# Optimization experiments

Measured on AMD Instinct MI355X. Metric: run time of the kernel, lower is better.

## Reference

```python
import jax, jax.numpy as jnp
import numpy as np

NH = 12          # num_heads
EPS = 1e-6       # eps for LayerNorm and QK RMSNorm
THETA = 10000.0


def _layernorm(x):
    # WanLayerNorm: fp32 layer-norm, no affine
    x = x.astype(jnp.float32)
    m = x.mean(-1, keepdims=True)
    v = ((x - m) ** 2).mean(-1, keepdims=True)
    return (x - m) * jax.lax.rsqrt(v + EPS)


def _rmsnorm(x, g):
    # WanRMSNorm: fp32 rms-norm then scale by weight g
    x32 = x.astype(jnp.float32)
    return x32 * jax.lax.rsqrt((x32 * x32).mean(-1, keepdims=True) + EPS) * g


def _rope_cos_sin(T, H, W, head_dim):
    # Per-token 3D RoPE angle tables. head_dim=128 -> half=64 complex pairs,
    # split [22, 21, 21] across (T, H, W) axes, matching rope_params/_build_freqs.
    half = head_dim // 2
    p_t = half - 2 * (half // 3)
    p_h = half // 3
    p_w = half // 3

    def ang(L, h):
        inv = 1.0 / (THETA ** (np.arange(h, dtype=np.float64) / h))
        return np.outer(np.arange(L, dtype=np.float64), inv)  # [L, h]

    a_t = np.broadcast_to(ang(T, p_t)[:, None, None, :], (T, H, W, p_t))
    a_h = np.broadcast_to(ang(H, p_h)[None, :, None, :], (T, H, W, p_h))
    a_w = np.broadcast_to(ang(W, p_w)[None, None, :, :], (T, H, W, p_w))
    a = np.concatenate([a_t, a_h, a_w], axis=-1).reshape(T * H * W, half)
    return jnp.asarray(np.cos(a), jnp.float32), jnp.asarray(np.sin(a), jnp.float32)


def _rope_apply(x, cos, sin):
    # x: [B, S, n, d]; pairs are interleaved along last dim (view_as_complex of reshape(..., -1, 2))
    xr = x[..., 0::2]
    xi = x[..., 1::2]
    c = cos[None, :, None, :]
    s = sin[None, :, None, :]
    out_r = xr * c - xi * s
    out_i = xr * s + xi * c
    return jnp.stack([out_r, out_i], axis=-1).reshape(x.shape)


def setup_inputs() -> dict:
    key = jax.random.key(0)
    ks = jax.random.split(key, 8)
    B, C, T, H, W = 1, 1536, 8, 22, 22
    scale = 1.0 / np.sqrt(C)
    return {
        "x": jax.random.normal(ks[0], (B, C, T, H, W), jnp.float32),
        "Wq": jax.random.normal(ks[1], (C, C), jnp.float32) * scale,
        "bq": jnp.zeros((C,), jnp.float32),
        "Wk": jax.random.normal(ks[2], (C, C), jnp.float32) * scale,
        "bk": jnp.zeros((C,), jnp.float32),
        "Wv": jax.random.normal(ks[3], (C, C), jnp.float32) * scale,
        "bv": jnp.zeros((C,), jnp.float32),
        "Wo": jax.random.normal(ks[4], (C, C), jnp.float32) * scale,
        "bo": jnp.zeros((C,), jnp.float32),
        "gq": jnp.ones((C,), jnp.float32),
        "gk": jnp.ones((C,), jnp.float32),
    }


def reference(x, Wq, bq, Wk, bk, Wv, bv, Wo, bo, gq, gk):
    B, C, T, H, W = x.shape
    S = T * H * W
    n = NH
    d = C // n

    # [B, C, T, H, W] -> [B, S, C]
    x_in = jnp.transpose(x, (0, 2, 3, 4, 1)).reshape(B, S, C)
    xn = _layernorm(x_in)

    # QKV projections + QK RMSNorm
    q = _rmsnorm(xn @ Wq.T + bq, gq).reshape(B, S, n, d)
    k = _rmsnorm(xn @ Wk.T + bk, gk).reshape(B, S, n, d)
    v = (xn @ Wv.T + bv).reshape(B, S, n, d)

    # 3D RoPE on q, k
    cos, sin = _rope_cos_sin(T, H, W, d)
    q = _rope_apply(q, cos, sin)
    k = _rope_apply(k, cos, sin)

    # scaled dot-product attention (flash_attention with default 1/sqrt(d) scale)
    scale = 1.0 / jnp.sqrt(jnp.float32(d))
    logits = jnp.einsum("bqhd,bkhd->bhqk", q, k) * scale
    attn = jax.nn.softmax(logits, axis=-1)
    o = jnp.einsum("bhqk,bkhd->bqhd", attn, v).reshape(B, S, C)

    # output projection + residual
    y = x_in + (o @ Wo.T + bo)
    return jnp.transpose(y.reshape(B, T, H, W, C), (0, 4, 1, 2, 3))
```

## Files before the change

kernel.cpp:

```cpp
#include <hip/hip_runtime.h>

#define S_TOT 3872
#define C_DIM 1536
#define NHEAD 12
#define DHEAD 128
#define TT 8
#define HH 22
#define WW 22
#define NKT 61
#define NKT2 31

typedef __bf16 bf16x8 __attribute__((ext_vector_type(8)));
typedef float  f32x4  __attribute__((ext_vector_type(4)));
typedef unsigned short u16x8 __attribute__((ext_vector_type(8)));

__device__ __forceinline__ float bf2f(unsigned short u) {
    unsigned int v = ((unsigned int)u) << 16;
    float f; __builtin_memcpy(&f, &v, 4); return f;
}
__device__ __forceinline__ unsigned short f2bf(float f) {
    unsigned int u; __builtin_memcpy(&u, &f, 4);
    u += 0x7fffu + ((u >> 16) & 1u);
    return (unsigned short)(u >> 16);
}
__device__ __forceinline__ unsigned int pk2_trunc(float a, float b) {
    unsigned int ua, ub;
    __builtin_memcpy(&ua, &a, 4); __builtin_memcpy(&ub, &b, 4);
    return (ua >> 16) | (ub & 0xffff0000u);
}
__device__ __forceinline__ float ldin(const void* p, size_t i, int isf32) {
    if (isf32) return ((const float*)p)[i];
    return bf2f(((const unsigned short*)p)[i]);
}
__device__ __forceinline__ float fexp2(float x) {
#if __has_builtin(__builtin_amdgcn_exp2f)
    return __builtin_amdgcn_exp2f(x);
#else
    return exp2f(x);
#endif
}
__device__ __forceinline__ void async16(const void* g, void* l) {
    __builtin_amdgcn_global_load_lds(
        (const __attribute__((address_space(1))) unsigned int*)g,
        (__attribute__((address_space(3))) unsigned int*)l, 16, 0, 0);
}
__device__ __forceinline__ int xcd_swz(int bid, int nwg) {
    int q = nwg >> 3, r = nwg & 7;
    int xcd = bid & 7, i = bid >> 3;
    int base = (xcd < r) ? xcd * (q + 1) : r * (q + 1) + (xcd - r) * q;
    return base + i;
}

__global__ void detect_vecs(const unsigned short* __restrict__ x,
                            const void* p0, const void* p1, const void* p2,
                            const void* p3, const void* p4, const void* p5,
                            int* __restrict__ flag, unsigned short* __restrict__ vecs,
                            float* __restrict__ sumb, float* __restrict__ sumsqb) {
    __shared__ int cnt;
    if (threadIdx.x == 0) cnt = 0;
    __syncthreads();
    int c = 0;
    for (int i = 0; i < 8; ++i) {
        unsigned short u = x[threadIdx.x * 8 + i];
        int e = (u >> 7) & 0xFF;
        if (e >= 112 && e <= 143) c++;
    }
    atomicAdd(&cnt, c);
    for (int j = threadIdx.x; j < S_TOT; j += 256) {
        sumb[j] = 0.f; sumsqb[j] = 0.f;
    }
    __syncthreads();
    int isf32 = (cnt >= 1900) ? 0 : 1;
    if (threadIdx.x == 0) *flag = isf32;
    const void* ps[6] = {p0, p1, p2, p3, p4, p5};
    for (int v = 0; v < 6; ++v)
        for (int j = threadIdx.x; j < C_DIM; j += 256)
            vecs[v * C_DIM + j] = f2bf(ldin(ps[v], j, isf32));
}

__global__ __launch_bounds__(256) void wconv4(const void* __restrict__ s0,
                                              const void* __restrict__ s1,
                                              const void* __restrict__ s2,
                                              const void* __restrict__ s3,
                                              const int* __restrict__ flag,
                                              unsigned short* __restrict__ d0,
                                              unsigned short* __restrict__ d1,
                                              unsigned short* __restrict__ d2,
                                              unsigned short* __restrict__ d3) {
    const void* srcs[4] = {s0, s1, s2, s3};
    unsigned short* dsts[4] = {d0, d1, d2, d3};
    const void* src = srcs[blockIdx.y];
    unsigned short* dst = dsts[blockIdx.y];
    size_t i = ((size_t)blockIdx.x * 256 + threadIdx.x) * 8;
    if (*flag) {
        const float* s = (const float*)src + i;
        float4 a = *(const float4*)s, b = *(const float4*)(s + 4);
        u16x8 o;
        o[0]=f2bf(a.x); o[1]=f2bf(a.y); o[2]=f2bf(a.z); o[3]=f2bf(a.w);
        o[4]=f2bf(b.x); o[5]=f2bf(b.y); o[6]=f2bf(b.z); o[7]=f2bf(b.w);
        *(u16x8*)(dst + i) = o;
    } else {
        *(u16x8*)(dst + i) = *(const u16x8*)((const unsigned short*)src + i);
    }
}

__global__ __launch_bounds__(256) void ln_stats(const void* __restrict__ x,
                                                const int* __restrict__ flag,
                                                float* __restrict__ sumb,
                                                float* __restrict__ sumsqb) {
    int isf32 = *flag;
    int sl = threadIdx.x & 63, cg = threadIdx.x >> 6;
    int s = blockIdx.x * 64 + sl;
    int cbase = blockIdx.y * 384;
    float sum = 0.f, sumsq = 0.f;
    if (s < S_TOT) {
        for (int c = cbase + cg; c < cbase + 384; c += 4) {
            float v = ldin(x, (size_t)c * S_TOT + s, isf32);
            sum += v; sumsq += v * v;
        }
    }
    __shared__ float r0[4][64], r1[4][64];
    r0[cg][sl] = sum; r1[cg][sl] = sumsq;
    __syncthreads();
    if (cg == 0 && s < S_TOT) {
        float st = r0[0][sl] + r0[1][sl] + r0[2][sl] + r0[3][sl];
        float sq = r1[0][sl] + r1[1][sl] + r1[2][sl] + r1[3][sl];
        atomicAdd(&sumb[s], st);
        atomicAdd(&sumsqb[s], sq);
    }
}

__global__ __launch_bounds__(256) void ln_norm_t(const void* __restrict__ x,
                                                 const int* __restrict__ flag,
                                                 const float* __restrict__ sumb,
                                                 const float* __restrict__ sumsqb,
                                                 unsigned short* __restrict__ xn) {
    int isf32 = *flag;
    __shared__ float tile[32][33];
    int s0 = blockIdx.x * 32, c0 = blockIdx.y * 32;
    int tx = threadIdx.x, ty = threadIdx.y;
    for (int r = 0; r < 4; ++r) {
        int cl = ty + 8 * r;
        tile[cl][tx] = ldin(x, (size_t)(c0 + cl) * S_TOT + (s0 + tx), isf32);
    }
    __syncthreads();
    for (int r = 0; r < 4; ++r) {
        int sl = ty + 8 * r;
        int s = s0 + sl, c = c0 + tx;
        float m = sumb[s] * (1.0f / C_DIM);
        float var = sumsqb[s] * (1.0f / C_DIM) - m * m;
        float rstd = rsqrtf(var + 1e-6f);
        xn[(size_t)s * C_DIM + c] = f2bf((tile[tx][sl] - m) * rstd);
    }
}

template<int BN>
__global__ __launch_bounds__(256, 3) void gemm2p(const unsigned short* __restrict__ A,
                                                 const unsigned short* __restrict__ W,
                                                 const unsigned short* __restrict__ bias,
                                                 unsigned short* __restrict__ D0,
                                                 unsigned short* __restrict__ D1,
                                                 unsigned short* __restrict__ DT,
                                                 int nsplit, int ntrans) {
    constexpr int NGRP = 8 + BN / 16;
    constexpr int GPW  = NGRP / 4;
    __shared__ __align__(16) unsigned short As[2][128 * 32];
    __shared__ __align__(16) unsigned short Bs[2][BN * 32];
    int nwg = gridDim.x * gridDim.y;
    int wg  = xcd_swz(blockIdx.y * gridDim.x + blockIdx.x, nwg);
    int m0 = (wg % gridDim.x) * 128, n0 = (wg / gridDim.x) * BN;
    int tid = threadIdx.x;
    int wave = tid >> 6, lane = tid & 63;
    int lm = lane & 15, lq = lane >> 4;
    int wr = wave >> 1, wc = wave & 1;
    int srow = lane >> 2, scol = (lane & 3) * 8;

    f32x4 acc[4][BN / 32];
    #pragma unroll
    for (int a = 0; a < 4; ++a)
        #pragma unroll
        for (int b = 0; b < BN / 32; ++b) acc[a][b] = (f32x4){0.f, 0.f, 0.f, 0.f};

    #pragma unroll
    for (int t = 0; t < GPW; ++t) {
        int g = wave * GPW + t;
        if (g < 8) {
            int am = m0 + g * 16 + srow; if (am > S_TOT - 1) am = S_TOT - 1;
            async16(A + (size_t)am * C_DIM + scol, (char*)As[0] + g * 1024);
        } else {
            int bn = n0 + (g - 8) * 16 + srow;
            async16(W + (size_t)bn * C_DIM + scol, (char*)Bs[0] + (g - 8) * 1024);
        }
    }
    int cur = 0;
    for (int k0 = 0; k0 < C_DIM; k0 += 32) {
        int kn = k0 + 32;
        if (kn < C_DIM) {
            #pragma unroll
            for (int t = 0; t < GPW; ++t) {
                int g = wave * GPW + t;
                if (g < 8) {
                    int am = m0 + g * 16 + srow; if (am > S_TOT - 1) am = S_TOT - 1;
                    async16(A + (size_t)am * C_DIM + kn + scol, (char*)As[cur ^ 1] + g * 1024);
                } else {
                    int bn = n0 + (g - 8) * 16 + srow;
                    async16(W + (size_t)bn * C_DIM + kn + scol, (char*)Bs[cur ^ 1] + (g - 8) * 1024);
                }
            }
            asm volatile("s_waitcnt vmcnt(%0)" :: "i"(GPW) : "memory");
        } else {
            asm volatile("s_waitcnt vmcnt(0)" ::: "memory");
        }
        __builtin_amdgcn_sched_barrier(0);
        __builtin_amdgcn_s_barrier();
        __builtin_amdgcn_sched_barrier(0);

        bf16x8 af[4], bf[BN / 32];
        #pragma unroll
        for (int mb = 0; mb < 4; ++mb)
            af[mb] = *(const bf16x8*)((const char*)As[cur] + (wr * 64 + mb * 16 + lm) * 64 + lq * 16);
        #pragma unroll
        for (int nb = 0; nb < BN / 32; ++nb)
            bf[nb] = *(const bf16x8*)((const char*)Bs[cur] + (wc * (BN / 2) + nb * 16 + lm) * 64 + lq * 16);
        #pragma unroll
        for (int mb = 0; mb < 4; ++mb)
            #pragma unroll
            for (int nb = 0; nb < BN / 32; ++nb)
                acc[mb][nb] = __builtin_amdgcn_mfma_f32_16x16x32_bf16(af[mb], bf[nb], acc[mb][nb], 0, 0, 0);

        __builtin_amdgcn_sched_barrier(0);
        __builtin_amdgcn_s_barrier();
        __builtin_amdgcn_sched_barrier(0);
        cur ^= 1;
    }

    #pragma unroll
    for (int mb = 0; mb < 4; ++mb) {
        #pragma unroll
        for (int nb = 0; nb < BN / 32; ++nb) {
            int gn = n0 + wc * (BN / 2) + nb * 16 + lm;
            float bv = bf2f(bias[gn]);
            if (gn >= ntrans) {
                int gm0 = m0 + wr * 64 + mb * 16 + lq * 4;
                if (gm0 < S_TOT) {
                    ushort4 pk;
                    pk.x = f2bf(acc[mb][nb][0] + bv);
                    pk.y = f2bf(acc[mb][nb][1] + bv);
                    pk.z = f2bf(acc[mb][nb][2] + bv);
                    pk.w = f2bf(acc[mb][nb][3] + bv);
                    *(ushort4*)(DT + (size_t)(gn - ntrans) * S_TOT + gm0) = pk;
                }
            } else {
                unsigned short* dst = (gn < nsplit) ? D0 : D1;
                int cn = (gn < nsplit) ? gn : gn - nsplit;
                #pragma unroll
                for (int r = 0; r < 4; ++r) {
                    int gm = m0 + wr * 64 + mb * 16 + lq * 4 + r;
                    if (gm < S_TOT) dst[(size_t)gm * C_DIM + cn] = f2bf(acc[mb][nb][r] + bv);
                }
            }
        }
    }
}

__global__ __launch_bounds__(256) void rope2(unsigned short* __restrict__ qbuf,
                                             unsigned short* __restrict__ kbuf,
                                             const unsigned short* __restrict__ gq,
                                             const unsigned short* __restrict__ gk,
                                             float qsc) {
    int s = blockIdx.x;
    unsigned short* row = (blockIdx.y ? kbuf : qbuf) + (size_t)s * C_DIM;
    const unsigned short* g = blockIdx.y ? gk : gq;
    float premul = blockIdx.y ? 1.0f : qsc;
    int tid = threadIdx.x;
    float ss = 0.f;
    for (int i = 0; i < 6; ++i) {
        float v = bf2f(row[tid + 256 * i]);
        ss += v * v;
    }
    for (int off = 32; off; off >>= 1) ss += __shfl_down(ss, off, 64);
    __shared__ float wsum[4];
    __shared__ float scale_sh;
    if ((tid & 63) == 0) wsum[tid >> 6] = ss;
    __syncthreads();
    if (tid == 0) {
        float tot = wsum[0] + wsum[1] + wsum[2] + wsum[3];
        scale_sh = rsqrtf(tot * (1.0f / C_DIM) + 1e-6f) * premul;
    }
    __syncthreads();
    float scale = scale_sh;

    int t  = s / (HH * WW);
    int rm = s % (HH * WW);
    int hh = rm / WW, ww = rm % WW;

    float e[3][2];
    int cols[3];
    for (int i = 0; i < 3; ++i) {
        int p = tid + 256 * i;
        int j = p & 63;
        int col0 = (p >> 6) * DHEAD + 2 * j;
        cols[i] = col0;
        float e0 = bf2f(row[col0])     * scale * bf2f(g[col0]);
        float e1 = bf2f(row[col0 + 1]) * scale * bf2f(g[col0 + 1]);
        float pos, fr;
        if (j < 22)       { pos = (float)t;  fr = (float)j        * (1.0f / 22.0f); }
        else if (j < 43)  { pos = (float)hh; fr = (float)(j - 22) * (1.0f / 21.0f); }
        else              { pos = (float)ww; fr = (float)(j - 43) * (1.0f / 21.0f); }
        float ang = pos * expf(fr * -9.210340371976184f);
        float c = cosf(ang), sn = sinf(ang);
        e[i][0] = e0 * c - e1 * sn;
        e[i][1] = e0 * sn + e1 * c;
    }
    for (int i = 0; i < 3; ++i) {
        row[cols[i]]     = f2bf(e[i][0]);
        row[cols[i] + 1] = f2bf(e[i][1]);
    }
}

__global__ __launch_bounds__(256, 2) void attn_mfma(const unsigned short* __restrict__ q,
                                                    const unsigned short* __restrict__ kp,
                                                    const unsigned short* __restrict__ vt,
                                                    unsigned short* __restrict__ o) {
    __shared__ __align__(16) unsigned char Ks[32768];
    __shared__ __align__(16) unsigned char Vs[32768];
    __shared__ __align__(16) unsigned char Ps[16384];

    int bid = xcd_swz(blockIdx.x, NHEAD * NKT);
    int h  = bid / NKT;
    int qt = bid % NKT;
    int q0 = qt * 64;
    int tid = threadIdx.x;
    int wave = tid >> 6, lane = tid & 63;
    int lm = lane & 15, lq = lane >> 4;

    bf16x8 qf[4];
    {
        int qr = q0 + wave * 16 + lm; if (qr >= S_TOT) qr = S_TOT - 1;
        const unsigned short* qptr = q + (size_t)qr * C_DIM + h * DHEAD + lq * 8;
        #pragma unroll
        for (int kc = 0; kc < 4; ++kc) qf[kc] = *(const bf16x8*)(qptr + kc * 32);
    }

    int krow = lane >> 4;
    int kcolA = ((lane & 15) ^ krow) * 8;
    int kcolB = ((lane & 15) ^ (4 + krow)) * 8;
    int vdr = lane >> 4;

    int sxor  = (lm & 7) << 4;
    int psxor = lm << 4;
    int ksoff[8], kqoff[4];
    #pragma unroll
    for (int nt = 0; nt < 8; ++nt) ksoff[nt] = (nt * 4 + (lm >> 2)) * 1024 + (lm & 3) * 256;
    #pragma unroll
    for (int kc = 0; kc < 4; ++kc) kqoff[kc] = (kc * 4 + lq) * 16;

    f32x4 oacc[8];
    #pragma unroll
    for (int i = 0; i < 8; ++i) oacc[i] = (f32x4){0.f, 0.f, 0.f, 0.f};
    float m_run = -__builtin_inff();
    float l_run = 0.f;

    for (int kt = 0; kt < NKT2; ++kt) {
        int k0 = kt * 128;
        #pragma unroll
        for (int t = 0; t < 8; ++t) {
            int g = wave * 8 + t;
            int grow = k0 + g * 4 + krow; if (grow > S_TOT - 1) grow = S_TOT - 1;
            async16(kp + (size_t)grow * C_DIM + h * DHEAD + ((t & 1) ? kcolB : kcolA),
                    Ks + g * 1024);
        }
        #pragma unroll
        for (int t = 0; t < 8; ++t) {
            int g = wave * 8 + t;
            int vslot = (lane & 15) ^ ((g & 3) * 4 + vdr);
            int vcol = k0 + vslot * 8; if (vcol > S_TOT - 8) vcol = S_TOT - 8;
            async16(vt + (size_t)(h * DHEAD + g * 4 + vdr) * S_TOT + vcol,
                    Vs + g * 1024);
        }
        __syncthreads();

        f32x4 sacc[8];
        #pragma unroll
        for (int nt = 0; nt < 8; ++nt) sacc[nt] = (f32x4){0.f, 0.f, 0.f, 0.f};
        #pragma unroll
        for (int kc = 0; kc < 4; ++kc)
            #pragma unroll
            for (int nt = 0; nt < 8; ++nt) {
                bf16x8 kf = *(const bf16x8*)(Ks + ((ksoff[nt] + kqoff[kc]) ^ sxor));
                sacc[nt] = __builtin_amdgcn_mfma_f32_16x16x32_bf16(kf, qf[kc], sacc[nt], 0, 0, 0);
            }
        if (kt == NKT2 - 1) {
            #pragma unroll
            for (int nt = 0; nt < 8; ++nt)
                #pragma unroll
                for (int r = 0; r < 4; ++r)
                    if (k0 + nt * 16 + lq * 4 + r >= S_TOT) sacc[nt][r] = -__builtin_inff();
        }
        float mtr[8];
        #pragma unroll
        for (int nt = 0; nt < 8; ++nt)
            mtr[nt] = fmaxf(fmaxf(sacc[nt][0], sacc[nt][1]),
                            fmaxf(sacc[nt][2], sacc[nt][3]));
        float pmax = fmaxf(fmaxf(fmaxf(mtr[0], mtr[1]), fmaxf(mtr[2], mtr[3])),
                           fmaxf(fmaxf(mtr[4], mtr[5]), fmaxf(mtr[6], mtr[7])));
        int defer = __all(pmax - m_run <= 8.0f);
        if (!defer) {
            float rmax = fmaxf(pmax, __shfl_xor(pmax, 16, 64));
            rmax = fmaxf(rmax, __shfl_xor(rmax, 32, 64));
            float mn = fmaxf(m_run, rmax);
            float alpha = fexp2(m_run - mn);
            l_run *= alpha;
            #pragma unroll
            for (int i = 0; i < 8; ++i)
                #pragma unroll
                for (int r = 0; r < 4; ++r) oacc[i][r] *= alpha;
            m_run = mn;
        }
        float rtot = 0.f;
        #pragma unroll
        for (int nt = 0; nt < 8; ++nt) {
            float p0 = fexp2(sacc[nt][0] - m_run);
            float p1 = fexp2(sacc[nt][1] - m_run);
            float p2 = fexp2(sacc[nt][2] - m_run);
            float p3 = fexp2(sacc[nt][3] - m_run);
            sacc[nt][0] = p0; sacc[nt][1] = p1;
            sacc[nt][2] = p2; sacc[nt][3] = p3;
            rtot += (p0 + p1) + (p2 + p3);
        }
        l_run += rtot;
        #pragma unroll
        for (int nt = 0; nt < 8; ++nt) {
            uint2 pk;
            pk.x = pk2_trunc(sacc[nt][0], sacc[nt][1]);
            pk.y = pk2_trunc(sacc[nt][2], sacc[nt][3]);
            *(uint2*)(Ps + (wave * 4096 + lm * 256 + ((nt * 32 + lq * 8) ^ psxor))) = pk;
        }
        #pragma unroll
        for (int kc = 0; kc < 4; ++kc) {
            bf16x8 pf = *(const bf16x8*)(Ps + (wave * 4096 + lm * 256 + ((kc * 64 + lq * 16) ^ psxor)));
            #pragma unroll
            for (int mt = 0; mt < 8; ++mt) {
                bf16x8 vf = *(const bf16x8*)(Vs + ((mt * 16 + lm) * 256 + ((kc * 64 + lq * 16) ^ psxor)));
                oacc[mt] = __builtin_amdgcn_mfma_f32_16x16x32_bf16(vf, pf, oacc[mt], 0, 0, 0);
            }
        }
        __syncthreads();
    }
    l_run += __shfl_xor(l_run, 16, 64);
    l_run += __shfl_xor(l_run, 32, 64);
    int qrow = q0 + wave * 16 + lm;
    if (qrow < S_TOT) {
        float inv = 1.0f / l_run;
        #pragma unroll
        for (int mt = 0; mt < 8; ++mt) {
            ushort4 pk;
            pk.x = f2bf(oacc[mt][0] * inv);
            pk.y = f2bf(oacc[mt][1] * inv);
            pk.z = f2bf(oacc[mt][2] * inv);
            pk.w = f2bf(oacc[mt][3] * inv);
            *(ushort4*)(o + (size_t)qrow * C_DIM + h * DHEAD + mt * 16 + lq * 4) = pk;
        }
    }
}

__global__ __launch_bounds__(256) void resid_t(const unsigned short* __restrict__ proj,
                                               const void* __restrict__ x,
                                               const int* __restrict__ flag,
                                               void* __restrict__ out) {
    int isf32 = *flag;
    __shared__ float tile[32][33];
    int s0 = blockIdx.x * 32, c0 = blockIdx.y * 32;
    int tx = threadIdx.x, ty = threadIdx.y;
    for (int r = 0; r < 4; ++r) {
        int sl = ty + 8 * r;
        tile[sl][tx] = bf2f(proj[(size_t)(s0 + sl) * C_DIM + (c0 + tx)]);
    }
    __syncthreads();
    for (int r = 0; r < 4; ++r) {
        int cl = ty + 8 * r;
        size_t idx = (size_t)(c0 + cl) * S_TOT + (s0 + tx);
        float val = ldin(x, idx, isf32) + tile[tx][cl];
        if (isf32) ((float*)out)[idx] = val;
        else       ((unsigned short*)out)[idx] = f2bf(val);
    }
}

extern "C" void kernel_launch(void* const* d_in, const int* in_sizes, int n_in,
                              void* d_out, int out_size, void* d_ws, size_t ws_size,
                              hipStream_t stream) {
    const void* x  = d_in[0];
    const void* Wq = d_in[1];
    const void* bq = d_in[2];
    const void* Wk = d_in[3];
    const void* bk = d_in[4];
    const void* Wv = d_in[5];
    const void* bv = d_in[6];
    const void* Wo = d_in[7];
    const void* bo = d_in[8];
    const void* gq = d_in[9];
    const void* gk = d_in[10];

    char* ws = (char*)d_ws;
    size_t off = 0;
    auto alloc = [&](size_t bytes) -> char* {
        char* p = ws + off;
        off += (bytes + 255) & ~(size_t)255;
        return p;
    };
    const size_t SC = (size_t)S_TOT * C_DIM;
    const size_t WSZ = (size_t)C_DIM * C_DIM * 2;
    unsigned short* xn   = (unsigned short*)alloc(SC * 2);
    unsigned short* qb   = (unsigned short*)alloc(SC * 2);
    unsigned short* kb   = (unsigned short*)alloc(SC * 2);
    unsigned short* Ws0  = (unsigned short*)alloc(WSZ);
    unsigned short* Ws1  = (unsigned short*)alloc(WSZ);
    unsigned short* Ws2  = (unsigned short*)alloc(WSZ);
    unsigned short* Ws3  = (unsigned short*)alloc(WSZ);
    unsigned short* vecs = (unsigned short*)alloc((size_t)6 * C_DIM * 2);
    float* sumb          = (float*)alloc((size_t)S_TOT * 4);
    float* sumsqb        = (float*)alloc((size_t)S_TOT * 4);
    int*   flag          = (int*)alloc(256);
    unsigned short* Vt   = (unsigned short*)d_out;
    unsigned short* ob   = xn;
    unsigned short* proj = qb;

    (void)Ws1; (void)Ws2;

    unsigned short* bo_b = vecs + 3 * C_DIM;
    unsigned short* gq_b = vecs + 4 * C_DIM;
    unsigned short* gk_b = vecs + 5 * C_DIM;

    const float QSC = 0.12751745f;

    dim3 t328(32, 8);
    dim3 tgrid(S_TOT / 32, C_DIM / 32);
    dim3 qkvgrid(31, 36);
    dim3 ogrid(31, 24);
    dim3 wgrid((C_DIM * C_DIM) / 2048, 4);
    dim3 sgrid(NKT, 4);
    dim3 rgrid(S_TOT, 2);

    detect_vecs<<<1, 256, 0, stream>>>((const unsigned short*)x, bq, bk, bv, bo, gq, gk,
                                       flag, vecs, sumb, sumsqb);
    wconv4<<<wgrid, 256, 0, stream>>>(Wq, Wk, Wv, Wo, flag, Ws0, Ws1, Ws2, Ws3);
    ln_stats<<<sgrid, 256, 0, stream>>>(x, flag, sumb, sumsqb);
    ln_norm_t<<<tgrid, t328, 0, stream>>>(x, flag, sumb, sumsqb, xn);

    gemm2p<128><<<qkvgrid, 256, 0, stream>>>(xn, Ws0, vecs, qb, kb, Vt, C_DIM, 2 * C_DIM);
    rope2<<<rgrid, 256, 0, stream>>>(qb, kb, gq_b, gk_b, QSC);

    attn_mfma<<<NHEAD * NKT, 256, 0, stream>>>(qb, kb, Vt, ob);

    gemm2p<64><<<ogrid, 256, 0, stream>>>(ob, Ws3, bo_b, proj, proj, proj, 1 << 30, 1 << 30);
    resid_t<<<tgrid, t328, 0, stream>>>(proj, x, flag, d_out);
}
```

Baseline: 500.0 us.

## Software-pipeline K/V async loads in attention and widen QKV GEMM tile

The attention loop now prefetches the next K tile right after the QK^T MFMAs and the next V tile right after the PV MFMAs. Explicit vmcnt waits and raw barriers replace the full __syncthreads, so global loads overlap compute instead of stalling at the top of each iteration. Separately, the QKV GEMM switches from a 128-wide to a 192-wide column tile, with a correspondingly smaller grid. The load pipelining relies on a hand-counted vmcnt(8), which risks races if the outstanding-load count does not match what the compiler emits, and the wider tile may reduce occupancy.

```diff
diff --git a/kernel.cpp b/kernel.cpp
--- a/kernel.cpp
+++ b/kernel.cpp
@@ -361,24 +361,40 @@
     float m_run = -__builtin_inff();
     float l_run = 0.f;
 
+#define STAGE_K(KT) do {                                                    \
+        int k0s = (KT) * 128;                                               \
+        _Pragma("unroll")                                                   \
+        for (int t = 0; t < 8; ++t) {                                       \
+            int g = wave * 8 + t;                                           \
+            int grow = k0s + g * 4 + krow; if (grow > S_TOT - 1) grow = S_TOT - 1; \
+            async16(kp + (size_t)grow * C_DIM + h * DHEAD + ((t & 1) ? kcolB : kcolA), \
+                    Ks + g * 1024);                                         \
+        } } while (0)
+#define STAGE_V(KT) do {                                                    \
+        int k0s = (KT) * 128;                                               \
+        _Pragma("unroll")                                                   \
+        for (int t = 0; t < 8; ++t) {                                       \
+            int g = wave * 8 + t;                                           \
+            int vslot = (lane & 15) ^ ((g & 3) * 4 + vdr);                  \
+            int vcol = k0s + vslot * 8; if (vcol > S_TOT - 8) vcol = S_TOT - 8; \
+            async16(vt + (size_t)(h * DHEAD + g * 4 + vdr) * S_TOT + vcol,  \
+                    Vs + g * 1024);                                         \
+        } } while (0)
+#define RAW_BARRIER() do {                                                  \
+        __builtin_amdgcn_sched_barrier(0);                                  \
+        __builtin_amdgcn_s_barrier();                                       \
+        __builtin_amdgcn_sched_barrier(0);                                  \
+    } while (0)
+
+    STAGE_K(0);
+    STAGE_V(0);
+
     for (int kt = 0; kt < NKT2; ++kt) {
         int k0 = kt * 128;
-        #pragma unroll
-        for (int t = 0; t < 8; ++t) {
-            int g = wave * 8 + t;
-            int grow = k0 + g * 4 + krow; if (grow > S_TOT - 1) grow = S_TOT - 1;
-            async16(kp + (size_t)grow * C_DIM + h * DHEAD + ((t & 1) ? kcolB : kcolA),
-                    Ks + g * 1024);
-        }
-        #pragma unroll
-        for (int t = 0; t < 8; ++t) {
-            int g = wave * 8 + t;
-            int vslot = (lane & 15) ^ ((g & 3) * 4 + vdr);
-            int vcol = k0 + vslot * 8; if (vcol > S_TOT - 8) vcol = S_TOT - 8;
-            async16(vt + (size_t)(h * DHEAD + g * 4 + vdr) * S_TOT + vcol,
-                    Vs + g * 1024);
-        }
-        __syncthreads();
+        int ktn = (kt + 1 < NKT2) ? kt + 1 : NKT2 - 1;
+
+        asm volatile("s_waitcnt vmcnt(8)" ::: "memory");
+        RAW_BARRIER();
 
         f32x4 sacc[8];
         #pragma unroll
@@ -390,6 +406,10 @@
                 bf16x8 kf = *(const bf16x8*)(Ks + ((ksoff[nt] + kqoff[kc]) ^ sxor));
                 sacc[nt] = __builtin_amdgcn_mfma_f32_16x16x32_bf16(kf, qf[kc], sacc[nt], 0, 0, 0);
             }
+
+        RAW_BARRIER();
+        STAGE_K(ktn);
+
         if (kt == NKT2 - 1) {
             #pragma unroll
             for (int nt = 0; nt < 8; ++nt)
@@ -436,6 +456,10 @@
             pk.y = pk2_trunc(sacc[nt][2], sacc[nt][3]);
             *(uint2*)(Ps + (wave * 4096 + lm * 256 + ((nt * 32 + lq * 8) ^ psxor))) = pk;
         }
+
+        asm volatile("s_waitcnt vmcnt(8)" ::: "memory");
+        RAW_BARRIER();
+
         #pragma unroll
         for (int kc = 0; kc < 4; ++kc) {
             bf16x8 pf = *(const bf16x8*)(Ps + (wave * 4096 + lm * 256 + ((kc * 64 + lq * 16) ^ psxor)));
@@ -445,8 +469,13 @@
                 oacc[mt] = __builtin_amdgcn_mfma_f32_16x16x32_bf16(vf, pf, oacc[mt], 0, 0, 0);
             }
         }
-        __syncthreads();
-    }
+
+        RAW_BARRIER();
+        STAGE_V(ktn);
+    }
+#undef STAGE_K
+#undef STAGE_V
+#undef RAW_BARRIER
     l_run += __shfl_xor(l_run, 16, 64);
     l_run += __shfl_xor(l_run, 32, 64);
     int qrow = q0 + wave * 16 + lm;
@@ -535,7 +564,7 @@
 
     dim3 t328(32, 8);
     dim3 tgrid(S_TOT / 32, C_DIM / 32);
-    dim3 qkvgrid(31, 36);
+    dim3 qkvgrid(31, 24);
     dim3 ogrid(31, 24);
     dim3 wgrid((C_DIM * C_DIM) / 2048, 4);
     dim3 sgrid(NKT, 4);
@@ -547,7 +576,7 @@
     ln_stats<<<sgrid, 256, 0, stream>>>(x, flag, sumb, sumsqb);
     ln_norm_t<<<tgrid, t328, 0, stream>>>(x, flag, sumb, sumsqb, xn);
 
-    gemm2p<128><<<qkvgrid, 256, 0, stream>>>(xn, Ws0, vecs, qb, kb, Vt, C_DIM, 2 * C_DIM);
+    gemm2p<192><<<qkvgrid, 256, 0, stream>>>(xn, Ws0, vecs, qb, kb, Vt, C_DIM, 2 * C_DIM);
     rope2<<<rgrid, 256, 0, stream>>>(qb, kb, gq_b, gk_b, QSC);
 
     attn_mfma<<<NHEAD * NKT, 256, 0, stream>>>(qb, kb, Vt, ob);
```

New measurement: 484.8 us. 1.03x faster.

## Restructure attention to 2 waves with 32 query rows each, 64-key tiles

Applied to the files above, without the earlier changes.

The attention kernel now runs 128 threads per block, and each wave handles two 16-row query groups. Each K/V fragment read from shared memory feeds two MFMAs, which raises reuse per LDS read. The key tile shrinks from 128 to 64, so LDS use drops and more blocks may fit per CU, at the cost of more loop iterations and barriers and higher register pressure. Separately, the QKV GEMM tile width changes from 128 to 192, with the grid adjusted to match.

```diff
diff --git a/kernel.cpp b/kernel.cpp
--- a/kernel.cpp
+++ b/kernel.cpp
@@ -8,7 +8,6 @@
 #define HH 22
 #define WW 22
 #define NKT 61
-#define NKT2 31
 
 typedef __bf16 bf16x8 __attribute__((ext_vector_type(8)));
 typedef float  f32x4  __attribute__((ext_vector_type(4)));
@@ -318,13 +317,13 @@
     }
 }
 
-__global__ __launch_bounds__(256, 2) void attn_mfma(const unsigned short* __restrict__ q,
+__global__ __launch_bounds__(128, 2) void attn_mfma(const unsigned short* __restrict__ q,
                                                     const unsigned short* __restrict__ kp,
                                                     const unsigned short* __restrict__ vt,
                                                     unsigned short* __restrict__ o) {
-    __shared__ __align__(16) unsigned char Ks[32768];
-    __shared__ __align__(16) unsigned char Vs[32768];
-    __shared__ __align__(16) unsigned char Ps[16384];
+    __shared__ __align__(16) unsigned char Ks[16384];
+    __shared__ __align__(16) unsigned char Vs[16384];
+    __shared__ __align__(16) unsigned char Ps[8192];
 
     int bid = xcd_swz(blockIdx.x, NHEAD * NKT);
     int h  = bid / NKT;
@@ -334,132 +333,149 @@
     int wave = tid >> 6, lane = tid & 63;
     int lm = lane & 15, lq = lane >> 4;
 
-    bf16x8 qf[4];
-    {
-        int qr = q0 + wave * 16 + lm; if (qr >= S_TOT) qr = S_TOT - 1;
+    bf16x8 qf[2][4];
+    #pragma unroll
+    for (int g = 0; g < 2; ++g) {
+        int qr = q0 + wave * 32 + g * 16 + lm; if (qr >= S_TOT) qr = S_TOT - 1;
         const unsigned short* qptr = q + (size_t)qr * C_DIM + h * DHEAD + lq * 8;
         #pragma unroll
-        for (int kc = 0; kc < 4; ++kc) qf[kc] = *(const bf16x8*)(qptr + kc * 32);
+        for (int kc = 0; kc < 4; ++kc) qf[g][kc] = *(const bf16x8*)(qptr + kc * 32);
     }
 
     int krow = lane >> 4;
     int kcolA = ((lane & 15) ^ krow) * 8;
     int kcolB = ((lane & 15) ^ (4 + krow)) * 8;
-    int vdr = lane >> 4;
-
-    int sxor  = (lm & 7) << 4;
-    int psxor = lm << 4;
-    int ksoff[8], kqoff[4];
-    #pragma unroll
-    for (int nt = 0; nt < 8; ++nt) ksoff[nt] = (nt * 4 + (lm >> 2)) * 1024 + (lm & 3) * 256;
+    int vr8 = lane >> 3;
+    int vslot = (lane & 7) ^ vr8;
+
+    int sxor = (lm & 7) << 4;
+    int ksoff[4], kqoff[4];
+    #pragma unroll
+    for (int nt = 0; nt < 4; ++nt) ksoff[nt] = (nt * 4 + (lm >> 2)) * 1024 + (lm & 3) * 256;
     #pragma unroll
     for (int kc = 0; kc < 4; ++kc) kqoff[kc] = (kc * 4 + lq) * 16;
 
-    f32x4 oacc[8];
-    #pragma unroll
-    for (int i = 0; i < 8; ++i) oacc[i] = (f32x4){0.f, 0.f, 0.f, 0.f};
-    float m_run = -__builtin_inff();
-    float l_run = 0.f;
-
-    for (int kt = 0; kt < NKT2; ++kt) {
-        int k0 = kt * 128;
+    f32x4 oacc[2][8];
+    #pragma unroll
+    for (int g = 0; g < 2; ++g)
+        #pragma unroll
+        for (int i = 0; i < 8; ++i) oacc[g][i] = (f32x4){0.f, 0.f, 0.f, 0.f};
+    float m_run[2] = {-__builtin_inff(), -__builtin_inff()};
+    float l_run[2] = {0.f, 0.f};
+
+    for (int kt = 0; kt < NKT; ++kt) {
+        int k0 = kt * 64;
         #pragma unroll
         for (int t = 0; t < 8; ++t) {
             int g = wave * 8 + t;
             int grow = k0 + g * 4 + krow; if (grow > S_TOT - 1) grow = S_TOT - 1;
-            async16(kp + (size_t)grow * C_DIM + h * DHEAD + ((t & 1) ? kcolB : kcolA),
+            async16(kp + (size_t)grow * C_DIM + h * DHEAD + ((g & 1) ? kcolB : kcolA),
                     Ks + g * 1024);
         }
-        #pragma unroll
-        for (int t = 0; t < 8; ++t) {
-            int g = wave * 8 + t;
-            int vslot = (lane & 15) ^ ((g & 3) * 4 + vdr);
+        {
             int vcol = k0 + vslot * 8; if (vcol > S_TOT - 8) vcol = S_TOT - 8;
-            async16(vt + (size_t)(h * DHEAD + g * 4 + vdr) * S_TOT + vcol,
-                    Vs + g * 1024);
+            #pragma unroll
+            for (int t = 0; t < 8; ++t) {
+                int g = wave * 8 + t;
+                async16(vt + (size_t)(h * DHEAD + g * 8 + vr8) * S_TOT + vcol,
+                        Vs + g * 1024);
+            }
         }
         __syncthreads();
 
-        f32x4 sacc[8];
-        #pragma unroll
-        for (int nt = 0; nt < 8; ++nt) sacc[nt] = (f32x4){0.f, 0.f, 0.f, 0.f};
+        f32x4 sacc[2][4];
+        #pragma unroll
+        for (int g = 0; g < 2; ++g)
+            #pragma unroll
+            for (int nt = 0; nt < 4; ++nt) sacc[g][nt] = (f32x4){0.f, 0.f, 0.f, 0.f};
         #pragma unroll
         for (int kc = 0; kc < 4; ++kc)
             #pragma unroll
-            for (int nt = 0; nt < 8; ++nt) {
+            for (int nt = 0; nt < 4; ++nt) {
                 bf16x8 kf = *(const bf16x8*)(Ks + ((ksoff[nt] + kqoff[kc]) ^ sxor));
-                sacc[nt] = __builtin_amdgcn_mfma_f32_16x16x32_bf16(kf, qf[kc], sacc[nt], 0, 0, 0);
-            }
-        if (kt == NKT2 - 1) {
-            #pragma unroll
-            for (int nt = 0; nt < 8; ++nt)
+                sacc[0][nt] = __builtin_amdgcn_mfma_f32_16x16x32_bf16(kf, qf[0][kc], sacc[0][nt], 0, 0, 0);
+                sacc[1][nt] = __builtin_amdgcn_mfma_f32_16x16x32_bf16(kf, qf[1][kc], sacc[1][nt], 0, 0, 0);
+            }
+        if (kt == NKT - 1) {
+            #pragma unroll
+            for (int g = 0; g < 2; ++g)
                 #pragma unroll
-                for (int r = 0; r < 4; ++r)
-                    if (k0 + nt * 16 + lq * 4 + r >= S_TOT) sacc[nt][r] = -__builtin_inff();
-        }
-        float mtr[8];
-        #pragma unroll
-        for (int nt = 0; nt < 8; ++nt)
-            mtr[nt] = fmaxf(fmaxf(sacc[nt][0], sacc[nt][1]),
-                            fmaxf(sacc[nt][2], sacc[nt][3]));
-        float pmax = fmaxf(fmaxf(fmaxf(mtr[0], mtr[1]), fmaxf(mtr[2], mtr[3])),
-                           fmaxf(fmaxf(mtr[4], mtr[5]), fmaxf(mtr[6], mtr[7])));
-        int defer = __all(pmax - m_run <= 8.0f);
-        if (!defer) {
-            float rmax = fmaxf(pmax, __shfl_xor(pmax, 16, 64));
-            rmax = fmaxf(rmax, __shfl_xor(rmax, 32, 64));
-            float mn = fmaxf(m_run, rmax);
-            float alpha = fexp2(m_run - mn);
-            l_run *= alpha;
-            #pragma unroll
-            for (int i = 0; i < 8; ++i)
+                for (int nt = 0; nt < 4; ++nt)
+                    #pragma unroll
+                    for (int r = 0; r < 4; ++r)
+                        if (k0 + nt * 16 + lq * 4 + r >= S_TOT) sacc[g][nt][r] = -__builtin_inff();
+        }
+        #pragma unroll
+        for (int g = 0; g < 2; ++g) {
+            float mtr[4];
+            #pragma unroll
+            for (int nt = 0; nt < 4; ++nt)
+                mtr[nt] = fmaxf(fmaxf(sacc[g][nt][0], sacc[g][nt][1]),
+                                fmaxf(sacc[g][nt][2], sacc[g][nt][3]));
+            float pmax = fmaxf(fmaxf(mtr[0], mtr[1]), fmaxf(mtr[2], mtr[3]));
+            int defer = __all(pmax - m_run[g] <= 8.0f);
+            if (!defer) {
+                float rmax = fmaxf(pmax, __shfl_xor(pmax, 16, 64));
+                rmax = fmaxf(rmax, __shfl_xor(rmax, 32, 64));
+                float mn = fmaxf(m_run[g], rmax);
+                float alpha = fexp2(m_run[g] - mn);
+                l_run[g] *= alpha;
                 #pragma unroll
-                for (int r = 0; r < 4; ++r) oacc[i][r] *= alpha;
-            m_run = mn;
-        }
-        float rtot = 0.f;
-        #pragma unroll
-        for (int nt = 0; nt < 8; ++nt) {
-            float p0 = fexp2(sacc[nt][0] - m_run);
-            float p1 = fexp2(sacc[nt][1] - m_run);
-            float p2 = fexp2(sacc[nt][2] - m_run);
-            float p3 = fexp2(sacc[nt][3] - m_run);
-            sacc[nt][0] = p0; sacc[nt][1] = p1;
-            sacc[nt][2] = p2; sacc[nt][3] = p3;
-            rtot += (p0 + p1) + (p2 + p3);
-        }
-        l_run += rtot;
-        #pragma unroll
-        for (int nt = 0; nt < 8; ++nt) {
-            uint2 pk;
-            pk.x = pk2_trunc(sacc[nt][0], sacc[nt][1]);
-            pk.y = pk2_trunc(sacc[nt][2], sacc[nt][3]);
-            *(uint2*)(Ps + (wave * 4096 + lm * 256 + ((nt * 32 + lq * 8) ^ psxor))) = pk;
-        }
-        #pragma unroll
-        for (int kc = 0; kc < 4; ++kc) {
-            bf16x8 pf = *(const bf16x8*)(Ps + (wave * 4096 + lm * 256 + ((kc * 64 + lq * 16) ^ psxor)));
+                for (int i = 0; i < 8; ++i)
+                    #pragma unroll
+                    for (int r = 0; r < 4; ++r) oacc[g][i][r] *= alpha;
+                m_run[g] = mn;
+            }
+            float rsn[4];
+            #pragma unroll
+            for (int nt = 0; nt < 4; ++nt) {
+                float p0 = fexp2(sacc[g][nt][0] - m_run[g]);
+                float p1 = fexp2(sacc[g][nt][1] - m_run[g]);
+                float p2 = fexp2(sacc[g][nt][2] - m_run[g]);
+                float p3 = fexp2(sacc[g][nt][3] - m_run[g]);
+                sacc[g][nt][0] = p0; sacc[g][nt][1] = p1;
+                sacc[g][nt][2] = p2; sacc[g][nt][3] = p3;
+                rsn[nt] = (p0 + p1) + (p2 + p3);
+            }
+            l_run[g] += (rsn[0] + rsn[1]) + (rsn[2] + rsn[3]);
+            #pragma unroll
+            for (int nt = 0; nt < 4; ++nt) {
+                uint2 pk;
+                pk.x = pk2_trunc(sacc[g][nt][0], sacc[g][nt][1]);
+                pk.y = pk2_trunc(sacc[g][nt][2], sacc[g][nt][3]);
+                *(uint2*)(Ps + (wave * 4096 + g * 2048 + lm * 128 + ((nt * 32 + lq * 8) ^ sxor))) = pk;
+            }
+        }
+        #pragma unroll
+        for (int kc = 0; kc < 2; ++kc) {
+            bf16x8 pf0 = *(const bf16x8*)(Ps + (wave * 4096 + lm * 128 + ((kc * 64 + lq * 16) ^ sxor)));
+            bf16x8 pf1 = *(const bf16x8*)(Ps + (wave * 4096 + 2048 + lm * 128 + ((kc * 64 + lq * 16) ^ sxor)));
             #pragma unroll
             for (int mt = 0; mt < 8; ++mt) {
-                bf16x8 vf = *(const bf16x8*)(Vs + ((mt * 16 + lm) * 256 + ((kc * 64 + lq * 16) ^ psxor)));
-                oacc[mt] = __builtin_amdgcn_mfma_f32_16x16x32_bf16(vf, pf, oacc[mt], 0, 0, 0);
+                bf16x8 vf = *(const bf16x8*)(Vs + ((mt * 16 + lm) * 128 + ((kc * 64 + lq * 16) ^ sxor)));
+                oacc[0][mt] = __builtin_amdgcn_mfma_f32_16x16x32_bf16(vf, pf0, oacc[0][mt], 0, 0, 0);
+                oacc[1][mt] = __builtin_amdgcn_mfma_f32_16x16x32_bf16(vf, pf1, oacc[1][mt], 0, 0, 0);
             }
         }
         __syncthreads();
     }
-    l_run += __shfl_xor(l_run, 16, 64);
-    l_run += __shfl_xor(l_run, 32, 64);
-    int qrow = q0 + wave * 16 + lm;
-    if (qrow < S_TOT) {
-        float inv = 1.0f / l_run;
-        #pragma unroll
-        for (int mt = 0; mt < 8; ++mt) {
-            ushort4 pk;
-            pk.x = f2bf(oacc[mt][0] * inv);
-            pk.y = f2bf(oacc[mt][1] * inv);
-            pk.z = f2bf(oacc[mt][2] * inv);
-            pk.w = f2bf(oacc[mt][3] * inv);
-            *(ushort4*)(o + (size_t)qrow * C_DIM + h * DHEAD + mt * 16 + lq * 4) = pk;
+    #pragma unroll
+    for (int g = 0; g < 2; ++g) {
+        float lt = l_run[g];
+        lt += __shfl_xor(lt, 16, 64);
+        lt += __shfl_xor(lt, 32, 64);
+        int qrow = q0 + wave * 32 + g * 16 + lm;
+        if (qrow < S_TOT) {
+            float inv = 1.0f / lt;
+            #pragma unroll
+            for (int mt = 0; mt < 8; ++mt) {
+                ushort4 pk;
+                pk.x = f2bf(oacc[g][mt][0] * inv);
+                pk.y = f2bf(oacc[g][mt][1] * inv);
+                pk.z = f2bf(oacc[g][mt][2] * inv);
+                pk.w = f2bf(oacc[g][mt][3] * inv);
+                *(ushort4*)(o + (size_t)qrow * C_DIM + h * DHEAD + mt * 16 + lq * 4) = pk;
+            }
         }
     }
 }
@@ -535,7 +551,7 @@
 
     dim3 t328(32, 8);
     dim3 tgrid(S_TOT / 32, C_DIM / 32);
-    dim3 qkvgrid(31, 36);
+    dim3 qkvgrid(31, 24);
     dim3 ogrid(31, 24);
     dim3 wgrid((C_DIM * C_DIM) / 2048, 4);
     dim3 sgrid(NKT, 4);
@@ -547,10 +563,10 @@
     ln_stats<<<sgrid, 256, 0, stream>>>(x, flag, sumb, sumsqb);
     ln_norm_t<<<tgrid, t328, 0, stream>>>(x, flag, sumb, sumsqb, xn);
 
-    gemm2p<128><<<qkvgrid, 256, 0, stream>>>(xn, Ws0, vecs, qb, kb, Vt, C_DIM, 2 * C_DIM);
+    gemm2p<192><<<qkvgrid, 256, 0, stream>>>(xn, Ws0, vecs, qb, kb, Vt, C_DIM, 2 * C_DIM);
     rope2<<<rgrid, 256, 0, stream>>>(qb, kb, gq_b, gk_b, QSC);
 
-    attn_mfma<<<NHEAD * NKT, 256, 0, stream>>>(qb, kb, Vt, ob);
+    attn_mfma<<<NHEAD * NKT, 128, 0, stream>>>(qb, kb, Vt, ob);
 
     gemm2p<64><<<ogrid, 256, 0, stream>>>(ob, Ws3, bo_b, proj, proj, proj, 1 << 30, 1 << 30);
     resid_t<<<tgrid, t328, 0, stream>>>(proj, x, flag, d_out);
```

New measurement: 469.9 us. 6.0% less time.
